# Performance work log

Hardware: AMD Instinct MI355X
Metric: run time of the kernel (lower is better)

## Reference

```python
import jax, jax.numpy as jnp
import numpy as np

TEMP = 1.0  # softmax temperature (init kwarg)


def setup_inputs() -> dict:
    key = jax.random.key(0)
    k1, k2 = jax.random.split(key)
    two_n, d_model = 512, 256
    embeddings = jax.random.normal(k1, (two_n, d_model), dtype=jnp.float32)
    targets = jax.random.uniform(k2, (two_n, 1), dtype=jnp.float32)
    return {"embeddings": embeddings, "targets": targets}


def reference(embeddings, targets):
    # embeddings: [2N, d_model], targets: [2N, 1]
    two_n = embeddings.shape[0]
    # label distance d[i,j] = |t_i - t_j|
    d = jnp.abs(targets - targets.T)                                  # [2N, 2N]
    # exp similarity s[i,j] = exp(-||e_i - e_j||_2 / temp)
    diff = embeddings[:, None, :] - embeddings[None, :, :]            # [2N, 2N, d]
    s = jnp.exp(-jnp.linalg.norm(diff, axis=-1) / TEMP)               # [2N, 2N]
    off_diag = 1.0 - jnp.eye(two_n, dtype=s.dtype)                    # [2N, 2N]
    # mask3[i,k,j] = (d[i,j] >= d[i,k]) * (j != i)
    mask3 = (d[:, None, :] >= d[:, :, None]).astype(s.dtype) * off_diag[:, None, :]
    # denominator D[i,k] = sum_j mask3[i,k,j] * s[i,j]
    denom = jnp.einsum('ikj,ij->ik', mask3, s)                        # [2N, 2N]
    loss = jnp.log(s / denom) * off_diag
    return -jnp.sum(loss) / (two_n * (two_n - 1))
```

## Files before the change

kernel.cpp:

```cpp
#include <hip/hip_runtime.h>
#include <math.h>

#define TWO_N 512
#define DM    256
#define NT    256

#define OFF_TSORT 1048576
#define OFF_PERM  1050624
#define OFF_INV   1052672
#define OFF_BSUM  1054720

#define ACC4(acc, A, B) { float _d;                      \
    _d = (A).x - (B).x; acc += _d * _d;                  \
    _d = (A).y - (B).y; acc += _d * _d;                  \
    _d = (A).z - (B).z; acc += _d * _d;                  \
    _d = (A).w - (B).w; acc += _d * _d; }

__global__ __launch_bounds__(NT) void supcr_dist_sort(
    const float* __restrict__ E, const float* __restrict__ T,
    float* __restrict__ R, float* __restrict__ tsort,
    int* __restrict__ perm, int* __restrict__ inv)
{
    const int bid = blockIdx.x;
    const int t   = threadIdx.x;

    if (bid < 256) {
        __shared__ float4 As4[32 * 65];
        __shared__ float4 Bs4[32 * 65];
        const int it = bid >> 4, jt = bid & 15;
        const float4* __restrict__ E4 = reinterpret_cast<const float4*>(E);

        for (int idx = t; idx < 32 * 64; idx += NT) {
            const int row = idx >> 6, c4 = idx & 63;
            As4[row * 65 + c4] = E4[(it * 32 + row) * 64 + c4];
            Bs4[row * 65 + c4] = E4[(jt * 32 + row) * 64 + c4];
        }
        __syncthreads();

        const int ty = t >> 4, tx = t & 15;
        float a00 = 0.f, a01 = 0.f, a10 = 0.f, a11 = 0.f;
        #pragma unroll 8
        for (int k4 = 0; k4 < 64; ++k4) {
            const float4 a0 = As4[ty * 65 + k4];
            const float4 a1 = As4[(ty + 16) * 65 + k4];
            const float4 b0 = Bs4[tx * 65 + k4];
            const float4 b1 = Bs4[(tx + 16) * 65 + k4];
            ACC4(a00, a0, b0); ACC4(a01, a0, b1);
            ACC4(a10, a1, b0); ACC4(a11, a1, b1);
        }
        const int r0 = it * 32 + ty, r1 = r0 + 16;
        const int c0 = jt * 32 + tx, c1 = c0 + 16;
        R[r0 * TWO_N + c0] = sqrtf(a00);
        R[r0 * TWO_N + c1] = sqrtf(a01);
        R[r1 * TWO_N + c0] = sqrtf(a10);
        R[r1 * TWO_N + c1] = sqrtf(a11);
    } else {
        __shared__ float key[TWO_N];
        __shared__ int   pay[TWO_N];
        key[t] = T[t]; key[t + 256] = T[t + 256];
        pay[t] = t;    pay[t + 256] = t + 256;
        __syncthreads();
        for (int kk = 2; kk <= TWO_N; kk <<= 1) {
            for (int j = kk >> 1; j > 0; j >>= 1) {
                #pragma unroll
                for (int w = 0; w < 2; ++w) {
                    const int e = t + w * 256;
                    const int p = e ^ j;
                    if (p > e) {
                        const float a = key[e], b = key[p];
                        const int  pa = pay[e], pb = pay[p];
                        const bool up = ((e & kk) == 0);
                        if (up ? (a > b) : (a < b)) {
                            key[e] = b; key[p] = a;
                            pay[e] = pb; pay[p] = pa;
                        }
                    }
                }
                __syncthreads();
            }
        }
        tsort[t] = key[t];           tsort[t + 256] = key[t + 256];
        perm[t]  = pay[t];           perm[t + 256]  = pay[t + 256];
        inv[pay[t]] = t;             inv[pay[t + 256]] = t + 256;
    }
}

__global__ __launch_bounds__(NT) void supcr_rows(
    const float* __restrict__ T, const float* __restrict__ R,
    const float* __restrict__ tsort, const int* __restrict__ perm,
    const int* __restrict__ inv, double* __restrict__ bsums)
{
    const int i = blockIdx.x;
    const int t = threadIdx.x;

    __shared__ float  ts[TWO_N];
    __shared__ float  P[TWO_N];
    __shared__ double red[NT];

    const float ti = T[i];

    #pragma unroll
    for (int w = 0; w < 2; ++w) {
        const int m = t + w * 256;
        ts[m] = tsort[m];
        const int pj = perm[m];
        P[m] = (pj == i) ? 0.f : __expf(-R[(size_t)i * TWO_N + pj]);
    }
    __syncthreads();

    for (int off = 1; off < TWO_N; off <<= 1) {
        const float v0 = (t >= off)       ? P[t - off]       : 0.f;
        const float v1 = (t + 256 >= off) ? P[t + 256 - off] : 0.f;
        __syncthreads();
        P[t]       += v0;
        P[t + 256] += v1;
        __syncthreads();
    }

    const float Stot = P[TWO_N - 1];
    const int   mi   = inv[i];

    float local = 0.f;
    #pragma unroll
    for (int w = 0; w < 2; ++w) {
        const int k = t + w * 256;
        if (k == i) continue;
        const float theta = fabsf(ti - T[k]);
        const float rik   = R[(size_t)i * TWO_N + k];

        const int nl = mi + 1;
        int pos = 0;
        #pragma unroll
        for (int step = 512; step >= 1; step >>= 1) {
            const int np = pos + step;
            if (np <= nl && fabsf(ti - ts[np - 1]) >= theta) pos = np;
        }
        const int cl = nl - pos;

        const int nr = TWO_N - mi;
        int pr = 0;
        #pragma unroll
        for (int step = 512; step >= 1; step >>= 1) {
            const int np = pr + step;
            if (np <= nr && fabsf(ti - ts[mi + np - 1]) < theta) pr = np;
        }
        const int cr = pr;

        float inner = 0.f;
        const int L  = mi - cl + 1;
        const int Rr = mi + cr - 1;
        if (Rr >= L) inner = P[Rr] - ((L > 0) ? P[L - 1] : 0.f);
        const float denom = Stot - inner;
        local += -rik - logf(denom);
    }

    red[t] = (double)local;
    __syncthreads();
    for (int off = NT / 2; off > 0; off >>= 1) {
        if (t < off) red[t] += red[t + off];
        __syncthreads();
    }
    if (t == 0) bsums[i] = red[0];
}

__global__ __launch_bounds__(TWO_N) void supcr_finalize(
    const double* __restrict__ bsums, float* __restrict__ out)
{
    __shared__ double red[TWO_N];
    const int t = threadIdx.x;
    red[t] = bsums[t];
    __syncthreads();
    for (int off = TWO_N / 2; off > 0; off >>= 1) {
        if (t < off) red[t] += red[t + off];
        __syncthreads();
    }
    if (t == 0)
        out[0] = (float)(-red[0] / (double)((long long)TWO_N * (TWO_N - 1)));
}

extern "C" void kernel_launch(void* const* d_in, const int* in_sizes, int n_in,
                              void* d_out, int out_size, void* d_ws, size_t ws_size,
                              hipStream_t stream) {
    (void)in_sizes; (void)n_in; (void)out_size; (void)ws_size;
    const float* E = (const float*)d_in[0];
    const float* T = (const float*)d_in[1];
    float* out = (float*)d_out;

    char* ws = (char*)d_ws;
    float*  R      = (float*)(ws);
    float*  tsortp = (float*)(ws + OFF_TSORT);
    int*    permp  = (int*)(ws + OFF_PERM);
    int*    invp   = (int*)(ws + OFF_INV);
    double* bsums  = (double*)(ws + OFF_BSUM);

    supcr_dist_sort<<<257, NT, 0, stream>>>(E, T, R, tsortp, permp, invp);
    supcr_rows<<<TWO_N, NT, 0, stream>>>(T, R, tsortp, permp, invp, bsums);
    supcr_finalize<<<1, TWO_N, 0, stream>>>(bsums, out);
}
```

Baseline: 78.78 us.

## Fuse distance, rank-sort and row scan into one per-row kernel

```diff
diff --git a/kernel.cpp b/kernel.cpp
--- a/kernel.cpp
+++ b/kernel.cpp
@@ -5,107 +5,65 @@
 #define DM    256
 #define NT    256
 
-#define OFF_TSORT 1048576
-#define OFF_PERM  1050624
-#define OFF_INV   1052672
-#define OFF_BSUM  1054720
-
-#define ACC4(acc, A, B) { float _d;                      \
+#define ACCD(acc, A, B) { float _d;                      \
     _d = (A).x - (B).x; acc += _d * _d;                  \
     _d = (A).y - (B).y; acc += _d * _d;                  \
     _d = (A).z - (B).z; acc += _d * _d;                  \
     _d = (A).w - (B).w; acc += _d * _d; }
 
-__global__ __launch_bounds__(NT) void supcr_dist_sort(
+__global__ __launch_bounds__(NT) void supcr_row_fused(
     const float* __restrict__ E, const float* __restrict__ T,
-    float* __restrict__ R, float* __restrict__ tsort,
-    int* __restrict__ perm, int* __restrict__ inv)
-{
-    const int bid = blockIdx.x;
-    const int t   = threadIdx.x;
-
-    if (bid < 256) {
-        __shared__ float4 As4[32 * 65];
-        __shared__ float4 Bs4[32 * 65];
-        const int it = bid >> 4, jt = bid & 15;
-        const float4* __restrict__ E4 = reinterpret_cast<const float4*>(E);
-
-        for (int idx = t; idx < 32 * 64; idx += NT) {
-            const int row = idx >> 6, c4 = idx & 63;
-            As4[row * 65 + c4] = E4[(it * 32 + row) * 64 + c4];
-            Bs4[row * 65 + c4] = E4[(jt * 32 + row) * 64 + c4];
-        }
-        __syncthreads();
-
-        const int ty = t >> 4, tx = t & 15;
-        float a00 = 0.f, a01 = 0.f, a10 = 0.f, a11 = 0.f;
-        #pragma unroll 8
-        for (int k4 = 0; k4 < 64; ++k4) {
-            const float4 a0 = As4[ty * 65 + k4];
-            const float4 a1 = As4[(ty + 16) * 65 + k4];
-            const float4 b0 = Bs4[tx * 65 + k4];
-            const float4 b1 = Bs4[(tx + 16) * 65 + k4];
-            ACC4(a00, a0, b0); ACC4(a01, a0, b1);
-            ACC4(a10, a1, b0); ACC4(a11, a1, b1);
-        }
-        const int r0 = it * 32 + ty, r1 = r0 + 16;
-        const int c0 = jt * 32 + tx, c1 = c0 + 16;
-        R[r0 * TWO_N + c0] = sqrtf(a00);
-        R[r0 * TWO_N + c1] = sqrtf(a01);
-        R[r1 * TWO_N + c0] = sqrtf(a10);
-        R[r1 * TWO_N + c1] = sqrtf(a11);
-    } else {
-        __shared__ float key[TWO_N];
-        __shared__ int   pay[TWO_N];
-        key[t] = T[t]; key[t + 256] = T[t + 256];
-        pay[t] = t;    pay[t + 256] = t + 256;
-        __syncthreads();
-        for (int kk = 2; kk <= TWO_N; kk <<= 1) {
-            for (int j = kk >> 1; j > 0; j >>= 1) {
-                #pragma unroll
-                for (int w = 0; w < 2; ++w) {
-                    const int e = t + w * 256;
-                    const int p = e ^ j;
-                    if (p > e) {
-                        const float a = key[e], b = key[p];
-                        const int  pa = pay[e], pb = pay[p];
-                        const bool up = ((e & kk) == 0);
-                        if (up ? (a > b) : (a < b)) {
-                            key[e] = b; key[p] = a;
-                            pay[e] = pb; pay[p] = pa;
-                        }
-                    }
-                }
-                __syncthreads();
-            }
-        }
-        tsort[t] = key[t];           tsort[t + 256] = key[t + 256];
-        perm[t]  = pay[t];           perm[t + 256]  = pay[t + 256];
-        inv[pay[t]] = t;             inv[pay[t + 256]] = t + 256;
-    }
-}
-
-__global__ __launch_bounds__(NT) void supcr_rows(
-    const float* __restrict__ T, const float* __restrict__ R,
-    const float* __restrict__ tsort, const int* __restrict__ perm,
-    const int* __restrict__ inv, double* __restrict__ bsums)
+    double* __restrict__ bsums)
 {
     const int i = blockIdx.x;
     const int t = threadIdx.x;
 
+    __shared__ float4 ei4[DM / 4];
+    __shared__ float  Tsh[TWO_N];
     __shared__ float  ts[TWO_N];
     __shared__ float  P[TWO_N];
     __shared__ double red[NT];
+    __shared__ int    miS;
 
-    const float ti = T[i];
+    const float4* __restrict__ E4 = reinterpret_cast<const float4*>(E);
 
-    #pragma unroll
-    for (int w = 0; w < 2; ++w) {
-        const int m = t + w * 256;
-        ts[m] = tsort[m];
-        const int pj = perm[m];
-        P[m] = (pj == i) ? 0.f : __expf(-R[(size_t)i * TWO_N + pj]);
+    Tsh[t] = T[t]; Tsh[t + 256] = T[t + 256];
+    if (t < DM / 4) ei4[t] = E4[(size_t)i * (DM / 4) + t];
+    __syncthreads();
+
+    const int ja = t, jb = t + 256;
+
+    const float ta = Tsh[ja], tb = Tsh[jb];
+    int rka = 0, rkb = 0;
+    const float4* Tsh4 = reinterpret_cast<const float4*>(Tsh);
+    #pragma unroll 4
+    for (int j4 = 0; j4 < TWO_N / 4; ++j4) {
+        const float4 tv = Tsh4[j4];
+        const int b0 = 4 * j4, b1 = b0 + 1, b2 = b0 + 2, b3 = b0 + 3;
+        rka += (tv.x < ta) || (tv.x == ta && b0 < ja);
+        rka += (tv.y < ta) || (tv.y == ta && b1 < ja);
+        rka += (tv.z < ta) || (tv.z == ta && b2 < ja);
+        rka += (tv.w < ta) || (tv.w == ta && b3 < ja);
+        rkb += (tv.x < tb) || (tv.x == tb && b0 < jb);
+        rkb += (tv.y < tb) || (tv.y == tb && b1 < jb);
+        rkb += (tv.z < tb) || (tv.z == tb && b2 < jb);
+        rkb += (tv.w < tb) || (tv.w == tb && b3 < jb);
     }
+
+    float d2a = 0.f, d2b = 0.f;
+    #pragma unroll 8
+    for (int k4 = 0; k4 < DM / 4; ++k4) {
+        const float4 ev = ei4[k4];
+        const float4 av = E4[(size_t)ja * (DM / 4) + k4];
+        const float4 bv = E4[(size_t)jb * (DM / 4) + k4];
+        ACCD(d2a, ev, av); ACCD(d2b, ev, bv);
+    }
+    const float ra = sqrtf(d2a), rb = sqrtf(d2b);
+
+    ts[rka] = ta;  P[rka] = (ja == i) ? 0.f : __expf(-ra);
+    ts[rkb] = tb;  P[rkb] = (jb == i) ? 0.f : __expf(-rb);
+    if (ja == i) miS = rka;
+    if (jb == i) miS = rkb;
     __syncthreads();
 
     for (int off = 1; off < TWO_N; off <<= 1) {
@@ -118,15 +76,16 @@
     }
 
     const float Stot = P[TWO_N - 1];
-    const int   mi   = inv[i];
+    const int   mi   = miS;
+    const float ti   = Tsh[i];
 
     float local = 0.f;
     #pragma unroll
     for (int w = 0; w < 2; ++w) {
         const int k = t + w * 256;
         if (k == i) continue;
-        const float theta = fabsf(ti - T[k]);
-        const float rik   = R[(size_t)i * TWO_N + k];
+        const float theta = fabsf(ti - Tsh[k]);
+        const float rik   = (w == 0) ? ra : rb;
 
         const int nl = mi + 1;
         int pos = 0;
@@ -185,15 +144,8 @@
     const float* E = (const float*)d_in[0];
     const float* T = (const float*)d_in[1];
     float* out = (float*)d_out;
+    double* bsums = (double*)d_ws;
 
-    char* ws = (char*)d_ws;
-    float*  R      = (float*)(ws);
-    float*  tsortp = (float*)(ws + OFF_TSORT);
-    int*    permp  = (int*)(ws + OFF_PERM);
-    int*    invp   = (int*)(ws + OFF_INV);
-    double* bsums  = (double*)(ws + OFF_BSUM);
-
-    supcr_dist_sort<<<257, NT, 0, stream>>>(E, T, R, tsortp, permp, invp);
-    supcr_rows<<<TWO_N, NT, 0, stream>>>(T, R, tsortp, permp, invp, bsums);
+    supcr_row_fused<<<TWO_N, NT, 0, stream>>>(E, T, bsums);
     supcr_finalize<<<1, TWO_N, 0, stream>>>(bsums, out);
 }
```

Result: slower. 117.8 us (+49.5%).

## Use wavefront shuffles for row prefix scan and reduction, interleave binary searches

Applied to the files above, without the earlier changes.

```diff
diff --git a/kernel.cpp b/kernel.cpp
--- a/kernel.cpp
+++ b/kernel.cpp
@@ -90,77 +90,93 @@
     const float* __restrict__ tsort, const int* __restrict__ perm,
     const int* __restrict__ inv, double* __restrict__ bsums)
 {
-    const int i = blockIdx.x;
-    const int t = threadIdx.x;
+    const int i    = blockIdx.x;
+    const int t    = threadIdx.x;
+    const int lane = t & 63, wid = t >> 6;
 
     __shared__ float  ts[TWO_N];
     __shared__ float  P[TWO_N];
-    __shared__ double red[NT];
+    __shared__ float  wsum[8];
+    __shared__ double red4[4];
 
     const float ti = T[i];
-
-    #pragma unroll
-    for (int w = 0; w < 2; ++w) {
-        const int m = t + w * 256;
-        ts[m] = tsort[m];
-        const int pj = perm[m];
-        P[m] = (pj == i) ? 0.f : __expf(-R[(size_t)i * TWO_N + pj]);
-    }
-    __syncthreads();
-
-    for (int off = 1; off < TWO_N; off <<= 1) {
-        const float v0 = (t >= off)       ? P[t - off]       : 0.f;
-        const float v1 = (t + 256 >= off) ? P[t + 256 - off] : 0.f;
-        __syncthreads();
-        P[t]       += v0;
-        P[t + 256] += v1;
-        __syncthreads();
-    }
-
-    const float Stot = P[TWO_N - 1];
-    const int   mi   = inv[i];
-
-    float local = 0.f;
-    #pragma unroll
-    for (int w = 0; w < 2; ++w) {
-        const int k = t + w * 256;
-        if (k == i) continue;
-        const float theta = fabsf(ti - T[k]);
-        const float rik   = R[(size_t)i * TWO_N + k];
-
-        const int nl = mi + 1;
-        int pos = 0;
-        #pragma unroll
-        for (int step = 512; step >= 1; step >>= 1) {
-            const int np = pos + step;
-            if (np <= nl && fabsf(ti - ts[np - 1]) >= theta) pos = np;
-        }
-        const int cl = nl - pos;
-
-        const int nr = TWO_N - mi;
-        int pr = 0;
-        #pragma unroll
-        for (int step = 512; step >= 1; step >>= 1) {
-            const int np = pr + step;
-            if (np <= nr && fabsf(ti - ts[mi + np - 1]) < theta) pr = np;
-        }
-        const int cr = pr;
-
+    const int m0 = t, m1 = t + 256;
+
+    ts[m0] = tsort[m0];  ts[m1] = tsort[m1];
+    const int pj0 = perm[m0], pj1 = perm[m1];
+    float v0 = (pj0 == i) ? 0.f : __expf(-R[(size_t)i * TWO_N + pj0]);
+    float v1 = (pj1 == i) ? 0.f : __expf(-R[(size_t)i * TWO_N + pj1]);
+
+    #pragma unroll
+    for (int off = 1; off < 64; off <<= 1) {
+        const float u0 = __shfl_up(v0, off, 64);
+        const float u1 = __shfl_up(v1, off, 64);
+        if (lane >= off) { v0 += u0; v1 += u1; }
+    }
+    if (lane == 63) { wsum[wid] = v0; wsum[4 + wid] = v1; }
+    __syncthreads();
+
+    float b0 = 0.f, tot = 0.f;
+    #pragma unroll
+    for (int w = 0; w < 4; ++w) {
+        const float s = wsum[w];
+        tot += s;
+        if (w < wid) b0 += s;
+    }
+    float b1 = tot;
+    #pragma unroll
+    for (int w = 0; w < 4; ++w) {
+        const float s = wsum[4 + w];
+        tot += s;
+        if (w < wid) b1 += s;
+    }
+    P[m0] = v0 + b0;
+    P[m1] = v1 + b1;
+    const float Stot = tot;
+    __syncthreads();
+
+    const int mi = inv[i];
+    const int nl = mi + 1;
+    const int nr = TWO_N - mi;
+
+    const float theta0 = fabsf(ti - T[m0]);
+    const float theta1 = fabsf(ti - T[m1]);
+    const float rik0   = R[(size_t)i * TWO_N + m0];
+    const float rik1   = R[(size_t)i * TWO_N + m1];
+
+    int pos0 = 0, pr0 = 0, pos1 = 0, pr1 = 0;
+    #pragma unroll
+    for (int step = 512; step >= 1; step >>= 1) {
+        const int a0 = pos0 + step, c0 = pr0 + step;
+        const int a1 = pos1 + step, c1 = pr1 + step;
+        if (a0 <= nl && fabsf(ti - ts[a0 - 1])      >= theta0) pos0 = a0;
+        if (c0 <= nr && fabsf(ti - ts[mi + c0 - 1]) <  theta0) pr0  = c0;
+        if (a1 <= nl && fabsf(ti - ts[a1 - 1])      >= theta1) pos1 = a1;
+        if (c1 <= nr && fabsf(ti - ts[mi + c1 - 1]) <  theta1) pr1  = c1;
+    }
+
+    float lf = 0.f;
+    if (m0 != i) {
+        const int cl = nl - pos0, cr = pr0;
+        const int L = mi - cl + 1, Rr = mi + cr - 1;
         float inner = 0.f;
-        const int L  = mi - cl + 1;
-        const int Rr = mi + cr - 1;
         if (Rr >= L) inner = P[Rr] - ((L > 0) ? P[L - 1] : 0.f);
-        const float denom = Stot - inner;
-        local += -rik - logf(denom);
-    }
-
-    red[t] = (double)local;
-    __syncthreads();
-    for (int off = NT / 2; off > 0; off >>= 1) {
-        if (t < off) red[t] += red[t + off];
-        __syncthreads();
-    }
-    if (t == 0) bsums[i] = red[0];
+        lf += -rik0 - logf(Stot - inner);
+    }
+    if (m1 != i) {
+        const int cl = nl - pos1, cr = pr1;
+        const int L = mi - cl + 1, Rr = mi + cr - 1;
+        float inner = 0.f;
+        if (Rr >= L) inner = P[Rr] - ((L > 0) ? P[L - 1] : 0.f);
+        lf += -rik1 - logf(Stot - inner);
+    }
+
+    double ld = (double)lf;
+    #pragma unroll
+    for (int off = 32; off > 0; off >>= 1) ld += __shfl_down(ld, off, 64);
+    if (lane == 0) red4[wid] = ld;
+    __syncthreads();
+    if (t == 0) bsums[i] = red4[0] + red4[1] + red4[2] + red4[3];
 }
 
 __global__ __launch_bounds__(TWO_N) void supcr_finalize(
```

Measured after the change: 76.80 us, median of 2. 1.03x faster.
